# Optimization experiments

Measured on AMD Instinct MI355X. Metric: run time of the kernel, lower is better.

The kernel has to match this reference:

```python
import jax, jax.numpy as jnp
import numpy as np

B = 65536
N_FEATURES = 96
N_TOKENS = 32      # ceil(96/3)
DEPTH = 6
N_Q3_LAYERS = 6    # stem + 4 residual + 1 reduce (3to1)
N_CLASSES = 10


def setup_inputs() -> dict:
    key = jax.random.key(0)
    k1, k2, k3 = jax.random.split(key, 3)
    x_ = jax.random.normal(k1, (B, N_FEATURES), dtype=jnp.float32)
    # packed per-layer, per-block StronglyEntanglingLayers weights: (n_layers, n_tokens, depth, 3, 3)
    thetas = 0.01 * jax.random.normal(k2, (N_Q3_LAYERS, N_TOKENS, DEPTH, 3, 3), dtype=jnp.float32)
    w_cls = jax.random.normal(k3, (N_CLASSES, N_TOKENS), dtype=jnp.float32) / np.sqrt(N_TOKENS)
    b_cls = jnp.zeros((N_CLASSES,), dtype=jnp.float32)
    return {"x_": x_, "thetas": thetas, "w_cls": w_cls, "b_cls": b_cls}


def _rot(phi, theta, omega):
    """PennyLane Rot(phi,theta,omega) matrix, elementwise over leading dims -> (...,2,2) complex64."""
    ct = jnp.cos(0.5 * theta)
    st = jnp.sin(0.5 * theta)
    m00 = jnp.exp(-0.5j * (phi + omega)) * ct
    m01 = -jnp.exp(0.5j * (phi - omega)) * st
    m10 = jnp.exp(-0.5j * (phi - omega)) * st
    m11 = jnp.exp(0.5j * (phi + omega)) * ct
    return jnp.stack([jnp.stack([m00, m01], -1), jnp.stack([m10, m11], -1)], -2)


_EINS_1Q = ['kij,bkjmn->bkimn', 'kij,bkmjn->bkmin', 'kij,bkmnj->bkmni']


def _apply_1q(psi, U, w):
    # psi: (B,K,2,2,2); U: (K,2,2) one gate per block k
    return jnp.einsum(_EINS_1Q[w], U, psi)


def _apply_cnot(psi, c, t):
    cax = 2 + c
    p0 = jnp.take(psi, 0, axis=cax)
    p1 = jnp.take(psi, 1, axis=cax)
    tax = 2 + t - (1 if t > c else 0)  # target axis after removing control axis
    p1 = jnp.flip(p1, axis=tax)        # X on target where control=1
    return jnp.stack([p0, p1], axis=cax)


def _run_q3(x, W):
    """3-qubit circuits batched over (B, K) blocks.
    x: (B,K,3) angles; W: (K,depth,3,3) SEL weights. Returns <Z_0>,<Z_1>,<Z_2>: (B,K,3).
    AngleEmbedding(RY) on |000> gives a product state."""
    half = 0.5 * x
    amps = jnp.stack([jnp.cos(half), jnp.sin(half)], -1)  # (B,K,3,2)
    psi = jnp.einsum('bki,bkj,bkl->bkijl', amps[:, :, 0], amps[:, :, 1], amps[:, :, 2])
    psi = psi.astype(jnp.complex64)
    depth = W.shape[1]
    for l in range(depth):
        for w in range(3):
            U = _rot(W[:, l, w, 0], W[:, l, w, 1], W[:, l, w, 2])
            psi = _apply_1q(psi, U, w)
        r = (l % 2) + 1  # PennyLane default ranges for 3 wires: 1,2,1,2,...
        for w in range(3):
            psi = _apply_cnot(psi, w, (w + r) % 3)
    probs = psi.real ** 2 + psi.imag ** 2  # (B,K,2,2,2)
    zs = []
    for w in range(3):
        other = tuple(2 + i for i in range(3) if i != w)
        pm = probs.sum(axis=other)  # (B,K,2)
        zs.append(pm[..., 0] - pm[..., 1])
    return jnp.stack(zs, -1)


def reference(x_, thetas, w_cls, b_cls):
    Bsz = x_.shape[0]
    K = thetas.shape[1]
    padded = 3 * K
    tot = padded - x_.shape[1]
    pl = tot // 2
    H = jnp.pad(x_, ((0, 0), (pl, tot - pl)))  # (B, padded)
    # stem: mode='first' (contiguous blocks)
    H = _run_q3(H.reshape(Bsz, K, 3), thetas[0]).reshape(Bsz, padded)
    # residual layers: mode='fully' -> transpose block/position then re-chunk
    for l in range(1, thetas.shape[0] - 1):
        inp = H.reshape(Bsz, K, 3).transpose(0, 2, 1).reshape(Bsz, K, 3)
        H = _run_q3(inp, thetas[l]).reshape(Bsz, padded) + H
    # reduce: 3to1 per block -> <Z_0> only
    z = _run_q3(H.reshape(Bsz, K, 3), thetas[-1])[..., 0]  # (B, K)
    return z @ w_cls.T + b_cls
```

## Files before the change

kernel.cpp:

```cpp
#include <hip/hip_runtime.h>


#define INV2PI 0.15915494309189535f

typedef unsigned int u32;
typedef _Float16 hf2 __attribute__((ext_vector_type(2)));

#if __has_builtin(__builtin_amdgcn_fdot2)
#define HAVE_FDOT2 1
#else
#define HAVE_FDOT2 0
#endif

__device__ __forceinline__ float fdot2e(hf2 a, hf2 m, float acc) {
#if HAVE_FDOT2
  return __builtin_amdgcn_fdot2(a, m, acc, false);
#else
  return fmaf((float)a.x, (float)m.x, fmaf((float)a.y, (float)m.y, acc));
#endif
}

#if __has_builtin(__builtin_amdgcn_sinf)
__device__ __forceinline__ float hwsin(float r) { return __builtin_amdgcn_sinf(r); }
__device__ __forceinline__ float hwcos(float r) { return __builtin_amdgcn_cosf(r); }
#else
__device__ __forceinline__ float hwsin(float r) { return __sinf(r * 6.2831853071795865f); }
__device__ __forceinline__ float hwcos(float r) { return __cosf(r * 6.2831853071795865f); }
#endif

__device__ __forceinline__ hf2 pkrtz(float a, float b) {
#if __has_builtin(__builtin_amdgcn_cvt_pkrtz)
  return __builtin_bit_cast(hf2, __builtin_amdgcn_cvt_pkrtz(a, b));
#else
  hf2 v = {(_Float16)a, (_Float16)b};
  return v;
#endif
}

__device__ __forceinline__ u32 pk_sc(float hrev) {
  return __builtin_bit_cast(u32, pkrtz(hwsin(hrev), hwcos(hrev)));
}
__device__ __forceinline__ hf2 as_hf2(u32 v) { return __builtin_bit_cast(hf2, v); }

__global__ __launch_bounds__(64) void build_T(const float* __restrict__ thetas,
                                              hf2* __restrict__ Thp,
                                              hf2* __restrict__ T5) {
  const int l = blockIdx.x >> 5;
  const int k = blockIdx.x & 31;
  const int t = threadIdx.x;
  __shared__ float Ur[8][8], Ui[8][8];
  __shared__ float rem[3][8][8];
  __shared__ float tvs[3][27];

  if (t < 8) {
    const int col = t;
    float pr[8], pi[8];
#pragma unroll
    for (int j = 0; j < 8; ++j) { pr[j] = (j == col) ? 1.f : 0.f; pi[j] = 0.f; }
    const float* th = thetas + (size_t)(l * 32 + k) * 54;
#pragma unroll
    for (int d = 0; d < 6; ++d) {
#pragma unroll
      for (int w = 0; w < 3; ++w) {
        float phi = th[(d * 3 + w) * 3 + 0];
        float tht = th[(d * 3 + w) * 3 + 1];
        float omg = th[(d * 3 + w) * 3 + 2];
        float st, ct, sp, cp, sm, cm;
        __sincosf(0.5f * tht, &st, &ct);
        __sincosf(0.5f * (phi + omg), &sp, &cp);
        __sincosf(0.5f * (phi - omg), &sm, &cm);
        float m00r =  cp * ct, m00i = -sp * ct;
        float m01r = -cm * st, m01i = -sm * st;
        float m10r =  cm * st, m10i = -sm * st;
        float m11r =  cp * ct, m11i =  sp * ct;
        const int s = 4 >> w;
#pragma unroll
        for (int base = 0; base < 8; ++base) {
          if (base & s) continue;
          float ar = pr[base], ai = pi[base];
          float br = pr[base + s], bi = pi[base + s];
          pr[base]     = m00r * ar - m00i * ai + m01r * br - m01i * bi;
          pi[base]     = m00r * ai + m00i * ar + m01r * bi + m01i * br;
          pr[base + s] = m10r * ar - m10i * ai + m11r * br - m11i * bi;
          pi[base + s] = m10r * ai + m10i * ar + m11r * bi + m11i * br;
        }
      }
      const int r = (d & 1) + 1;
#pragma unroll
      for (int w = 0; w < 3; ++w) {
        const int cs = 4 >> w;
        const int ts = 4 >> ((w + r) % 3);
#pragma unroll
        for (int idx = 0; idx < 8; ++idx) {
          if (!(idx & cs) || (idx & ts)) continue;
          const int j2 = idx | ts;
          float tr = pr[idx]; pr[idx] = pr[j2]; pr[j2] = tr;
          float ti = pi[idx]; pi[idx] = pi[j2]; pi[j2] = ti;
        }
      }
    }
#pragma unroll
    for (int j = 0; j < 8; ++j) { Ur[col][j] = pr[j]; Ui[col][j] = pi[j]; }
  }
  __syncthreads();

  {
    const int a = t >> 3, bb = t & 7;
#pragma unroll
    for (int w = 0; w < 3; ++w) {
      float acc = 0.f;
#pragma unroll
      for (int c = 0; c < 8; ++c) {
        float zs = ((c >> (2 - w)) & 1) ? -1.f : 1.f;
        acc += zs * (Ur[a][c] * Ur[bb][c] + Ui[a][c] * Ui[bb][c]);
      }
      rem[w][a][bb] = acc;
    }
  }
  __syncthreads();

  {
    const int   ga[3][2] = {{0, 1}, {0, 1}, {0, 1}};
    const int   gb[3][2] = {{0, 1}, {0, 1}, {1, 0}};
    const float gc[3][2] = {{0.5f, 0.5f}, {0.5f, -0.5f}, {0.5f, 0.5f}};
    const int MONO[3][3] = {{0, 3, 4}, {1, 5, 6}, {2, 7, 8}};
    for (int e = t; e < 81; e += 64) {
      int w = e / 27, re = e % 27;
      int p = re / 9, q = (re % 9) / 3, r = re % 3;
      float acc = 0.f;
#pragma unroll
      for (int e0 = 0; e0 < 2; ++e0)
#pragma unroll
        for (int e1 = 0; e1 < 2; ++e1)
#pragma unroll
          for (int e2 = 0; e2 < 2; ++e2) {
            int a  = (ga[p][e0] << 2) | (ga[q][e1] << 1) | ga[r][e2];
            int bb = (gb[p][e0] << 2) | (gb[q][e1] << 1) | gb[r][e2];
            acc += gc[p][e0] * gc[q][e1] * gc[r][e2] * rem[w][a][bb];
          }
      tvs[w][p * 9 + MONO[q][r]] = acc;
    }
  }
  __syncthreads();

  if (l < 5) {
    if (t < 48) {
      int w = t >> 4, u = t & 15;
      hf2 v;
      if (u < 15) {
        int p = u / 5, d = u % 5;
        float lo = tvs[w][p * 9 + ((d == 4) ? 8 : 2 * d)] * INV2PI;
        float hi = (d == 4) ? 0.f : tvs[w][p * 9 + 2 * d + 1] * INV2PI;
        v = pkrtz(lo, hi);
      } else {
        v = pkrtz(0.f, 0.f);
      }
      Thp[((size_t)(l * 32 + k)) * 48 + w * 16 + u] = v;
    }
  } else {
    if (t < 16) {
      int u = t;
      hf2 v;
      if (u < 15) {
        int p = u / 5, d = u % 5;
        float lo = tvs[0][p * 9 + ((d == 4) ? 8 : 2 * d)];
        float hi = (d == 4) ? 0.f : tvs[0][p * 9 + 2 * d + 1];
        v = pkrtz(lo, hi);
      } else {
        v = pkrtz(0.f, 0.f);
      }
      T5[k * 16 + u] = v;
    }
  }
}

__device__ __forceinline__ void evalk_sc(const hf2* __restrict__ tb,
                                         u32 cw, u32 aw, u32 bw,
                                         float* __restrict__ z) {
  hf2 C = as_hf2(cw), A = as_hf2(aw), B = as_hf2(bw);
  hf2 Blo = __builtin_shufflevector(B, B, 0, 0);
  hf2 Bhi = __builtin_shufflevector(B, B, 1, 1);
  hf2 Pa = A * Blo;
  hf2 Pb = A * Bhi;
  const hf2 ONE2 = {(_Float16)1.0f, (_Float16)1.0f};
  const hf2 ZERO2 = {(_Float16)0.0f, (_Float16)0.0f};
  hf2 M0 = __builtin_shufflevector(ONE2, A, 0, 3);
  hf2 M1 = __builtin_shufflevector(A, B, 0, 3);
  hf2 M2 = __builtin_shufflevector(B, Pb, 0, 3);
  hf2 M3 = __builtin_shufflevector(Pa, Pb, 1, 2);
  hf2 M4 = __builtin_shufflevector(Pa, ZERO2, 0, 2);
  float s0 = (float)C.x, c0 = (float)C.y;
#pragma unroll
  for (int w = 0; w < 3; ++w) {
    const hf2* tw = tb + w * 16;
    float P[3];
#pragma unroll
    for (int p = 0; p < 3; ++p) {
      const hf2* tt = tw + p * 5;
      float acc = fdot2e(tt[0], M0, 0.0f);
      acc = fdot2e(tt[1], M1, acc);
      acc = fdot2e(tt[2], M2, acc);
      acc = fdot2e(tt[3], M3, acc);
      acc = fdot2e(tt[4], M4, acc);
      P[p] = acc;
    }
    z[w] = fmaf(s0, P[2], fmaf(c0, P[1], P[0]));
  }
}

__device__ __forceinline__ float evalk1(const hf2* __restrict__ tb,
                                        float a0, float a1, float a2) {
  float s0 = hwsin(a0), c0 = hwcos(a0);
  float s1 = hwsin(a1), c1 = hwcos(a1);
  float s2 = hwsin(a2), c2 = hwcos(a2);
  hf2 M0 = pkrtz(1.0f, c1);
  hf2 M1 = pkrtz(s1, c2);
  hf2 M2 = pkrtz(s2, c1 * c2);
  hf2 M3 = pkrtz(c1 * s2, s1 * c2);
  hf2 M4 = pkrtz(s1 * s2, 0.f);
  float P[3];
#pragma unroll
  for (int p = 0; p < 3; ++p) {
    const hf2* tt = tb + p * 5;
    float acc = fdot2e(tt[0], M0, 0.0f);
    acc = fdot2e(tt[1], M1, acc);
    acc = fdot2e(tt[2], M2, acc);
    acc = fdot2e(tt[3], M3, acc);
    acc = fdot2e(tt[4], M4, acc);
    P[p] = acc;
  }
  return fmaf(s0, P[2], fmaf(c0, P[1], P[0]));
}

__global__ __launch_bounds__(512, 8) void vqc_main(const float* __restrict__ x,
                                                   const hf2* __restrict__ Thp,
                                                   const hf2* __restrict__ T5,
                                                   const float* __restrict__ wcls,
                                                   const float* __restrict__ bcls,
                                                   float* __restrict__ out) {
  __shared__ u32 ex[64 * 100];
  const int t = threadIdx.x;
  const int b = t & 63;
  const int ws = __builtin_amdgcn_readfirstlane(t >> 6);
  const size_t b0 = (size_t)blockIdx.x * 64;

  const float4* xv = (const float4*)(x + b0 * 96);
#pragma unroll
  for (int i = 0; i < 3; ++i) {
    int f = t + i * 512;
    float4 v = xv[f];
    int d = 4 * f, row = d / 96, col = d % 96;
    uint4 pv;
    pv.x = pk_sc(v.x * INV2PI);
    pv.y = pk_sc(v.y * INV2PI);
    pv.z = pk_sc(v.z * INV2PI);
    pv.w = pk_sc(v.w * INV2PI);
    *(uint4*)&ex[row * 100 + col] = pv;
  }
  __syncthreads();

  float h[4][3];
  const int rb = b * 100 + 12 * ws;

#pragma unroll
  for (int l = 0; l < 5; ++l) {
    uint4 r0 = *(const uint4*)&ex[rb + 0];
    uint4 r1 = *(const uint4*)&ex[rb + 4];
    uint4 r2 = *(const uint4*)&ex[rb + 8];
    __syncthreads();
    const hf2* tb = Thp + ((size_t)l * 32 + 4 * ws) * 48;
    float z0[3], z1[3], z2[3], z3[3];
    evalk_sc(tb + 0 * 48, r0.x, r0.y, r0.z, z0);
    evalk_sc(tb + 1 * 48, r0.w, r1.x, r1.y, z1);
    evalk_sc(tb + 2 * 48, r1.z, r1.w, r2.x, z2);
    evalk_sc(tb + 3 * 48, r2.y, r2.z, r2.w, z3);
    if (l == 0) {
#pragma unroll
      for (int j = 0; j < 3; ++j) {
        h[0][j] = z0[j]; h[1][j] = z1[j]; h[2][j] = z2[j]; h[3][j] = z3[j];
      }
    } else {
#pragma unroll
      for (int j = 0; j < 3; ++j) {
        h[0][j] += z0[j]; h[1][j] += z1[j]; h[2][j] += z2[j]; h[3][j] += z3[j];
      }
    }
    if (l < 4) {
#pragma unroll
      for (int j = 0; j < 3; ++j) {
        uint4 wv;
        wv.x = pk_sc(h[0][j]);
        wv.y = pk_sc(h[1][j]);
        wv.z = pk_sc(h[2][j]);
        wv.w = pk_sc(h[3][j]);
        *(uint4*)&ex[b * 100 + 32 * j + 4 * ws] = wv;
      }
      __syncthreads();
    }
  }

  {
    float4 zv;
    zv.x = evalk1(T5 + (4 * ws + 0) * 16, h[0][0], h[0][1], h[0][2]);
    zv.y = evalk1(T5 + (4 * ws + 1) * 16, h[1][0], h[1][1], h[1][2]);
    zv.z = evalk1(T5 + (4 * ws + 2) * 16, h[2][0], h[2][1], h[2][2]);
    zv.w = evalk1(T5 + (4 * ws + 3) * 16, h[3][0], h[3][1], h[3][2]);
    *(float4*)&ex[b * 100 + 4 * ws] = zv;
  }
  __syncthreads();

  for (int idx = t; idx < 640; idx += 512) {
    int bb = idx / 10, c = idx % 10;
    float acc = bcls[c];
#pragma unroll
    for (int k = 0; k < 32; ++k)
      acc = fmaf(__uint_as_float(ex[bb * 100 + k]), wcls[c * 32 + k], acc);
    out[(b0 + bb) * 10 + c] = acc;
  }
}

extern "C" void kernel_launch(void* const* d_in, const int* in_sizes, int n_in,
                              void* d_out, int out_size, void* d_ws, size_t ws_size,
                              hipStream_t stream) {
  const float* x  = (const float*)d_in[0];
  const float* th = (const float*)d_in[1];
  const float* wc = (const float*)d_in[2];
  const float* bc = (const float*)d_in[3];
  float* out = (float*)d_out;
  hf2* Thp = (hf2*)d_ws;
  hf2* T5  = Thp + 5 * 32 * 48;

  build_T<<<192, 64, 0, stream>>>(th, Thp, T5);
  vqc_main<<<65536 / 64, 512, 0, stream>>>(x, Thp, T5, wc, bc, out);
}
```

Baseline: 46.43 us.

## Remap threads to one token per lane with LDS-staged tables and bpermute shuffles

Each thread now handles a single (sample, token) pair, 16 samples per block, instead of 4 tokens of one sample. The per-layer coefficient tables are staged into padded LDS and read from there rather than from global memory. The token transpose between residual layers is done with ds_bpermute inside a wavefront, which removes the block-wide barriers and the LDS exchange buffer. The cost is that every block reloads about 30KB of tables into LDS, and the grid grows to four times as many blocks. Input loads also become strided scalar reads instead of coalesced float4 loads.

New measurement: 67.99 us (median of 2 runs). 46.5% more time.

```diff
diff --git a/kernel.cpp b/kernel.cpp
--- a/kernel.cpp
+++ b/kernel.cpp
@@ -2,6 +2,8 @@
 
 
 #define INV2PI 0.15915494309189535f
+#define T_STRIDE 50
+#define T5_STRIDE 18
 
 typedef unsigned int u32;
 typedef _Float16 hf2 __attribute__((ext_vector_type(2)));
@@ -174,9 +176,14 @@
   }
 }
 
-__device__ __forceinline__ void evalk_sc(const hf2* __restrict__ tb,
-                                         u32 cw, u32 aw, u32 bw,
-                                         float* __restrict__ z) {
+__device__ __forceinline__ hf2 td(const uint2* __restrict__ ch, int n) {
+  u32 d = (n & 1) ? ch[n >> 1].y : ch[n >> 1].x;
+  return as_hf2(d);
+}
+
+__device__ __forceinline__ void evalk_r(const uint2* __restrict__ ch,
+                                        u32 cw, u32 aw, u32 bw,
+                                        float* __restrict__ z) {
   hf2 C = as_hf2(cw), A = as_hf2(aw), B = as_hf2(bw);
   hf2 Blo = __builtin_shufflevector(B, B, 0, 0);
   hf2 Bhi = __builtin_shufflevector(B, B, 1, 1);
@@ -192,24 +199,24 @@
   float s0 = (float)C.x, c0 = (float)C.y;
 #pragma unroll
   for (int w = 0; w < 3; ++w) {
-    const hf2* tw = tb + w * 16;
+    const int bdw = 16 * w;
     float P[3];
 #pragma unroll
     for (int p = 0; p < 3; ++p) {
-      const hf2* tt = tw + p * 5;
-      float acc = fdot2e(tt[0], M0, 0.0f);
-      acc = fdot2e(tt[1], M1, acc);
-      acc = fdot2e(tt[2], M2, acc);
-      acc = fdot2e(tt[3], M3, acc);
-      acc = fdot2e(tt[4], M4, acc);
+      const int o = bdw + p * 5;
+      float acc = fdot2e(td(ch, o + 0), M0, 0.0f);
+      acc = fdot2e(td(ch, o + 1), M1, acc);
+      acc = fdot2e(td(ch, o + 2), M2, acc);
+      acc = fdot2e(td(ch, o + 3), M3, acc);
+      acc = fdot2e(td(ch, o + 4), M4, acc);
       P[p] = acc;
     }
     z[w] = fmaf(s0, P[2], fmaf(c0, P[1], P[0]));
   }
 }
 
-__device__ __forceinline__ float evalk1(const hf2* __restrict__ tb,
-                                        float a0, float a1, float a2) {
+__device__ __forceinline__ float evalk1_r(const uint2* __restrict__ c5,
+                                          float a0, float a1, float a2) {
   float s0 = hwsin(a0), c0 = hwcos(a0);
   float s1 = hwsin(a1), c1 = hwcos(a1);
   float s2 = hwsin(a2), c2 = hwcos(a2);
@@ -221,101 +228,107 @@
   float P[3];
 #pragma unroll
   for (int p = 0; p < 3; ++p) {
-    const hf2* tt = tb + p * 5;
-    float acc = fdot2e(tt[0], M0, 0.0f);
-    acc = fdot2e(tt[1], M1, acc);
-    acc = fdot2e(tt[2], M2, acc);
-    acc = fdot2e(tt[3], M3, acc);
-    acc = fdot2e(tt[4], M4, acc);
+    const int o = p * 5;
+    float acc = fdot2e(td(c5, o + 0), M0, 0.0f);
+    acc = fdot2e(td(c5, o + 1), M1, acc);
+    acc = fdot2e(td(c5, o + 2), M2, acc);
+    acc = fdot2e(td(c5, o + 3), M3, acc);
+    acc = fdot2e(td(c5, o + 4), M4, acc);
     P[p] = acc;
   }
   return fmaf(s0, P[2], fmaf(c0, P[1], P[0]));
 }
 
-__global__ __launch_bounds__(512, 8) void vqc_main(const float* __restrict__ x,
+__global__ __launch_bounds__(512, 4) void vqc_main(const float* __restrict__ x,
                                                    const hf2* __restrict__ Thp,
                                                    const hf2* __restrict__ T5,
                                                    const float* __restrict__ wcls,
                                                    const float* __restrict__ bcls,
                                                    float* __restrict__ out) {
-  __shared__ u32 ex[64 * 100];
+  __shared__ u32 Tl[5 * 32 * T_STRIDE];
+  __shared__ u32 T5l[32 * T5_STRIDE];
+  __shared__ float zbuf[16 * 33];
   const int t = threadIdx.x;
-  const int b = t & 63;
-  const int ws = __builtin_amdgcn_readfirstlane(t >> 6);
-  const size_t b0 = (size_t)blockIdx.x * 64;
-
-  const float4* xv = (const float4*)(x + b0 * 96);
-#pragma unroll
-  for (int i = 0; i < 3; ++i) {
-    int f = t + i * 512;
-    float4 v = xv[f];
-    int d = 4 * f, row = d / 96, col = d % 96;
-    uint4 pv;
-    pv.x = pk_sc(v.x * INV2PI);
-    pv.y = pk_sc(v.y * INV2PI);
-    pv.z = pk_sc(v.z * INV2PI);
-    pv.w = pk_sc(v.w * INV2PI);
-    *(uint4*)&ex[row * 100 + col] = pv;
-  }
-  __syncthreads();
-
-  float h[4][3];
-  const int rb = b * 100 + 12 * ws;
-
+
+  const u32* Tg = (const u32*)Thp;
+  for (int g = t; g < 7680; g += 512) {
+    int lk = g / 48, c = g - lk * 48;
+    Tl[lk * T_STRIDE + c] = Tg[g];
+  }
+  {
+    const u32* T5g = (const u32*)T5;
+    int k5 = t >> 4, c5 = t & 15;
+    if (t < 512) T5l[k5 * T5_STRIDE + c5] = T5g[t];
+  }
+
+  const int lane = t & 63;
+  const int wv = t >> 6;
+  const int r2 = lane >> 5;
+  const int k = lane & 31;
+  const int row = (wv << 1) | r2;
+  const size_t grow = (size_t)blockIdx.x * 16 + row;
+
+  const float* xr = x + grow * 96 + 3 * k;
+  u32 w0 = pk_sc(xr[0] * INV2PI);
+  u32 w1 = pk_sc(xr[1] * INV2PI);
+  u32 w2 = pk_sc(xr[2] * INV2PI);
+
+  int addrj[3], jp[3];
+#pragma unroll
+  for (int j = 0; j < 3; ++j) {
+    int m = 3 * k + j;
+    addrj[j] = (((r2 << 5) | (m & 31)) << 2);
+    jp[j] = m >> 5;
+  }
+
+  __syncthreads();
+
+  float h[3];
 #pragma unroll
   for (int l = 0; l < 5; ++l) {
-    uint4 r0 = *(const uint4*)&ex[rb + 0];
-    uint4 r1 = *(const uint4*)&ex[rb + 4];
-    uint4 r2 = *(const uint4*)&ex[rb + 8];
-    __syncthreads();
-    const hf2* tb = Thp + ((size_t)l * 32 + 4 * ws) * 48;
-    float z0[3], z1[3], z2[3], z3[3];
-    evalk_sc(tb + 0 * 48, r0.x, r0.y, r0.z, z0);
-    evalk_sc(tb + 1 * 48, r0.w, r1.x, r1.y, z1);
-    evalk_sc(tb + 2 * 48, r1.z, r1.w, r2.x, z2);
-    evalk_sc(tb + 3 * 48, r2.y, r2.z, r2.w, z3);
+    const u32* tb = &Tl[(l * 32 + k) * T_STRIDE];
+    uint2 ch[24];
+#pragma unroll
+    for (int c2 = 0; c2 < 24; ++c2) ch[c2] = *(const uint2*)&tb[2 * c2];
+    float z[3];
+    evalk_r(ch, w0, w1, w2, z);
     if (l == 0) {
 #pragma unroll
+      for (int j = 0; j < 3; ++j) h[j] = z[j];
+    } else {
+#pragma unroll
+      for (int j = 0; j < 3; ++j) h[j] += z[j];
+    }
+    if (l < 4) {
+      u32 p0 = pk_sc(h[0]), p1 = pk_sc(h[1]), p2 = pk_sc(h[2]);
+      u32 nw[3];
+#pragma unroll
       for (int j = 0; j < 3; ++j) {
-        h[0][j] = z0[j]; h[1][j] = z1[j]; h[2][j] = z2[j]; h[3][j] = z3[j];
-      }
-    } else {
-#pragma unroll
-      for (int j = 0; j < 3; ++j) {
-        h[0][j] += z0[j]; h[1][j] += z1[j]; h[2][j] += z2[j]; h[3][j] += z3[j];
-      }
-    }
-    if (l < 4) {
-#pragma unroll
-      for (int j = 0; j < 3; ++j) {
-        uint4 wv;
-        wv.x = pk_sc(h[0][j]);
-        wv.y = pk_sc(h[1][j]);
-        wv.z = pk_sc(h[2][j]);
-        wv.w = pk_sc(h[3][j]);
-        *(uint4*)&ex[b * 100 + 32 * j + 4 * ws] = wv;
-      }
-      __syncthreads();
+        u32 v0 = __builtin_amdgcn_ds_bpermute(addrj[j], p0);
+        u32 v1 = __builtin_amdgcn_ds_bpermute(addrj[j], p1);
+        u32 v2 = __builtin_amdgcn_ds_bpermute(addrj[j], p2);
+        nw[j] = (jp[j] == 0) ? v0 : ((jp[j] == 1) ? v1 : v2);
+      }
+      w0 = nw[0]; w1 = nw[1]; w2 = nw[2];
     }
   }
 
   {
-    float4 zv;
-    zv.x = evalk1(T5 + (4 * ws + 0) * 16, h[0][0], h[0][1], h[0][2]);
-    zv.y = evalk1(T5 + (4 * ws + 1) * 16, h[1][0], h[1][1], h[1][2]);
-    zv.z = evalk1(T5 + (4 * ws + 2) * 16, h[2][0], h[2][1], h[2][2]);
-    zv.w = evalk1(T5 + (4 * ws + 3) * 16, h[3][0], h[3][1], h[3][2]);
-    *(float4*)&ex[b * 100 + 4 * ws] = zv;
-  }
-  __syncthreads();
-
-  for (int idx = t; idx < 640; idx += 512) {
-    int bb = idx / 10, c = idx % 10;
+    const u32* t5b = &T5l[k * T5_STRIDE];
+    uint2 c5[8];
+#pragma unroll
+    for (int c2 = 0; c2 < 8; ++c2) c5[c2] = *(const uint2*)&t5b[2 * c2];
+    zbuf[row * 33 + k] = evalk1_r(c5, h[0], h[1], h[2]);
+  }
+  __syncthreads();
+
+  if (t < 160) {
+    int bb = t / 10, c = t - bb * 10;
     float acc = bcls[c];
 #pragma unroll
-    for (int k = 0; k < 32; ++k)
-      acc = fmaf(__uint_as_float(ex[bb * 100 + k]), wcls[c * 32 + k], acc);
-    out[(b0 + bb) * 10 + c] = acc;
+    for (int k2 = 0; k2 < 32; ++k2)
+      acc = fmaf(zbuf[bb * 33 + k2], wcls[c * 32 + k2], acc);
+    out[((size_t)blockIdx.x * 16 + bb) * 10 + c] = acc;
   }
 }
 
@@ -331,5 +344,5 @@
   hf2* T5  = Thp + 5 * 32 * 48;
 
   build_T<<<192, 64, 0, stream>>>(th, Thp, T5);
-  vqc_main<<<65536 / 64, 512, 0, stream>>>(x, Thp, T5, wc, bc, out);
-}
+  vqc_main<<<65536 / 16, 512, 0, stream>>>(x, Thp, T5, wc, bc, out);
+}
```
